# Performance work log

Measured on AMD Instinct MI355X. Metric: run time of the kernel, lower is better.

The kernel has to match this reference:

```python
import jax, jax.numpy as jnp
import numpy as np

EPS_NORM = 1e-12
EPS_BN = 1e-5


def _normalize(x):
    n = jnp.linalg.norm(x, axis=-1, keepdims=True)
    return x / jnp.maximum(n, EPS_NORM)


def _bn_train(x, gamma, beta):
    # BatchNorm2d in training mode: stats over all dims except channel (last)
    mean = jnp.mean(x, axis=(0, 1, 2), keepdims=True)
    var = jnp.var(x, axis=(0, 1, 2), keepdims=True)
    return (x - mean) / jnp.sqrt(var + EPS_BN) * gamma + beta


def setup_inputs() -> dict:
    key = jax.random.key(0)
    ks = jax.random.split(key, 16)
    B, N, K, C = 2, 32768, 16, 64
    Cm = 32  # mlp output channels
    Wn = 16  # weightnet output channels
    xyz = jax.random.normal(ks[0], (B, N, 3), dtype=jnp.float32)
    feats = jax.random.normal(ks[1], (B, N, C), dtype=jnp.float32)
    nei_inds = jax.random.randint(ks[2], (B, N, K), 0, N, dtype=jnp.int32)
    xyz_norm = _normalize(jax.random.normal(ks[3], (B, N, 3), dtype=jnp.float32))
    s = 0.05
    return {
        "xyz": xyz, "feats": feats, "xyz_norm": xyz_norm, "nei_inds": nei_inds,
        # main MLP (1x1 convs, no BN since cfg.BATCH_NORM=False)
        "W_mlp1": jax.random.normal(ks[4], (Cm, C + 3), dtype=jnp.float32) * s,
        "b_mlp1": jnp.zeros((Cm,), dtype=jnp.float32),
        "W_mlp2": jax.random.normal(ks[5], (Cm, Cm), dtype=jnp.float32) * s,
        "b_mlp2": jnp.zeros((Cm,), dtype=jnp.float32),
        # weightnet: 12 -> 8 -> 8 -> 16, each conv1x1 + BN + relu
        "wn_W0": jax.random.normal(ks[6], (8, 12), dtype=jnp.float32) * s,
        "wn_b0": jnp.zeros((8,), dtype=jnp.float32),
        "wn_g0": jnp.ones((8,), dtype=jnp.float32),
        "wn_be0": jnp.zeros((8,), dtype=jnp.float32),
        "wn_W1": jax.random.normal(ks[7], (8, 8), dtype=jnp.float32) * s,
        "wn_b1": jnp.zeros((8,), dtype=jnp.float32),
        "wn_g1": jnp.ones((8,), dtype=jnp.float32),
        "wn_be1": jnp.zeros((8,), dtype=jnp.float32),
        "wn_W2": jax.random.normal(ks[8], (Wn, 8), dtype=jnp.float32) * s,
        "wn_b2": jnp.zeros((Wn,), dtype=jnp.float32),
        "wn_g2": jnp.ones((Wn,), dtype=jnp.float32),
        "wn_be2": jnp.zeros((Wn,), dtype=jnp.float32),
        # final linear: Cm*Wn -> C
        "W_lin": jax.random.normal(ks[9], (C, Cm * Wn), dtype=jnp.float32) * s,
        "b_lin": jnp.zeros((C,), dtype=jnp.float32),
    }


def reference(xyz, feats, xyz_norm, nei_inds,
              W_mlp1, b_mlp1, W_mlp2, b_mlp2,
              wn_W0, wn_b0, wn_g0, wn_be0,
              wn_W1, wn_b1, wn_g1, wn_be1,
              wn_W2, wn_b2, wn_g2, wn_be2,
              W_lin, b_lin):
    B, N, _ = xyz.shape
    K = nei_inds.shape[-1]
    bidx = jnp.arange(B)[:, None, None]
    # gathers
    g_xyz = xyz[bidx, nei_inds]          # [B,N,K,3]
    g_norm = xyz_norm[bidx, nei_inds]    # [B,N,K,3]
    g_feat = feats[bidx, nei_inds]       # [B,N,K,C]
    r_miu = g_xyz - xyz[:, :, None, :]   # localized_xyz
    n_miu = xyz_norm[:, :, None, :]      # [B,N,1,3]
    r_hat = _normalize(r_miu)
    # viewpoint-invariant frame
    dot_nm_rhat = jnp.sum(n_miu * r_hat, axis=-1, keepdims=True)
    v_miu = _normalize(n_miu - dot_nm_rhat * r_hat)
    w_miu = _normalize(jnp.cross(r_hat, v_miu))
    th1 = jnp.sum(g_norm * n_miu, axis=-1, keepdims=True)
    th2 = dot_nm_rhat
    th3 = jnp.sum(r_hat * g_norm, axis=-1, keepdims=True)
    th4 = jnp.sum(r_miu * n_miu, axis=-1, keepdims=True)
    th5 = th3
    th6 = jnp.sum(g_norm * v_miu, axis=-1, keepdims=True)
    th7 = jnp.sum(g_norm * w_miu, axis=-1, keepdims=True)
    th8 = jnp.sum(r_miu * jnp.cross(g_norm, jnp.broadcast_to(n_miu, g_norm.shape)),
                  axis=-1, keepdims=True)
    th9 = jnp.linalg.norm(r_miu, axis=-1, keepdims=True)
    wn_in = jnp.concatenate([th1, th2, th3, th4, th5, th6, th7, th8, th9, r_miu], axis=-1)  # [B,N,K,12]
    # feature MLP (1x1 convs, channels-last)
    h = jnp.concatenate([g_feat, r_miu], axis=-1)  # [B,N,K,C+3]
    h = jax.nn.relu(jnp.einsum('bnkc,oc->bnko', h, W_mlp1) + b_mlp1)
    h = jax.nn.relu(jnp.einsum('bnkc,oc->bnko', h, W_mlp2) + b_mlp2)  # [B,N,K,Cm]
    # weightnet (conv1x1 + BN(train) + relu)
    w = wn_in
    for Wc, bc, g, be in ((wn_W0, wn_b0, wn_g0, wn_be0),
                          (wn_W1, wn_b1, wn_g1, wn_be1),
                          (wn_W2, wn_b2, wn_g2, wn_be2)):
        w = jax.nn.relu(_bn_train(jnp.einsum('bnkc,oc->bnko', w, Wc) + bc, g, be))
    # PointConv aggregation over K: [B,N,Cm,Wn] -> flatten (Cm outer, Wn inner)
    agg = jnp.einsum('bnkc,bnkw->bncw', h, w).reshape(B, N, -1)
    out = jax.nn.relu(agg @ W_lin.T + b_lin) + feats
    return out
```

## Files before the change

### kernel.cpp

```cpp
#include <hip/hip_runtime.h>
#include <math.h>

#define BB 2
#define NN 32768
#define KK 16
#define CC 64
#define MTOT (BB*NN*KK)

typedef short short8 __attribute__((ext_vector_type(8)));
typedef float f32x4 __attribute__((ext_vector_type(4)));

static_assert(MTOT == 1048576, "size");

__device__ __forceinline__ float frsq(float x) { return __builtin_amdgcn_rsqf(x); }

__device__ __forceinline__ unsigned cvtpk(float lo, float hi) {
    unsigned r;
    asm("v_cvt_pk_bf16_f32 %0, %1, %2" : "=v"(r) : "v"(lo), "v"(hi));
    return r;
}

__device__ __forceinline__ short f2bf(float f) {
    union { float f; unsigned u; } c; c.f = f;
    const unsigned r = c.u + 0x7FFFu + ((c.u >> 16) & 1u);
    return (short)(r >> 16);
}

__device__ __forceinline__ float bf2f(unsigned short u) {
    union { unsigned u; float f; } c; c.u = ((unsigned)u) << 16; return c.f;
}

__device__ __forceinline__ f32x4 mfma16(short8 a, short8 b, f32x4 c) {
    return __builtin_amdgcn_mfma_f32_16x16x32_bf16(a, b, c, 0, 0, 0);
}

__device__ __forceinline__ void geom12(int s, const float* __restrict__ xyz,
                                       const float* __restrict__ xyzn,
                                       const int* __restrict__ nei, float* win) {
    const int pn = s >> 4;
    const int b  = pn >> 15;
    const int nj = nei[s];
    const size_t gj = (size_t)(b * NN + nj);

    const float cx = xyz[(size_t)pn*3],  cy = xyz[(size_t)pn*3+1],  cz = xyz[(size_t)pn*3+2];
    const float nmx = xyzn[(size_t)pn*3], nmy = xyzn[(size_t)pn*3+1], nmz = xyzn[(size_t)pn*3+2];
    const float gx = xyz[gj*3],  gy = xyz[gj*3+1],  gz = xyz[gj*3+2];
    const float gnx = xyzn[gj*3], gny = xyzn[gj*3+1], gnz = xyzn[gj*3+2];

    const float rx = gx - cx, ry = gy - cy, rz = gz - cz;
    const float ss = rx*rx + ry*ry + rz*rz;
    const float rinv = frsq(fmaxf(ss, 1e-24f));
    const float rlen = ss * rinv;
    const float rhx = rx*rinv, rhy = ry*rinv, rhz = rz*rinv;

    const float d_nr = nmx*rhx + nmy*rhy + nmz*rhz;
    float vx = nmx - d_nr*rhx, vy = nmy - d_nr*rhy, vz = nmz - d_nr*rhz;
    const float vinv = frsq(fmaxf(vx*vx + vy*vy + vz*vz, 1e-24f));
    vx *= vinv; vy *= vinv; vz *= vinv;

    float wx = rhy*vz - rhz*vy;
    float wy = rhz*vx - rhx*vz;
    float wz = rhx*vy - rhy*vx;
    const float winv = frsq(fmaxf(wx*wx + wy*wy + wz*wz, 1e-24f));
    wx *= winv; wy *= winv; wz *= winv;

    const float th1 = gnx*nmx + gny*nmy + gnz*nmz;
    const float th3 = rhx*gnx + rhy*gny + rhz*gnz;
    const float th4 = rx*nmx + ry*nmy + rz*nmz;
    const float th6 = gnx*vx + gny*vy + gnz*vz;
    const float th7 = gnx*wx + gny*wy + gnz*wz;
    const float ccx = gny*nmz - gnz*nmy;
    const float ccy = gnz*nmx - gnx*nmz;
    const float ccz = gnx*nmy - gny*nmx;
    const float th8 = rx*ccx + ry*ccy + rz*ccz;

    win[0]=th1; win[1]=d_nr; win[2]=th3; win[3]=th4; win[4]=th3; win[5]=th6;
    win[6]=th7; win[7]=th8; win[8]=rlen; win[9]=rx; win[10]=ry; win[11]=rz;
}

template<int ON, int IN>
__device__ __forceinline__ void lin(const float* a, const float* __restrict__ W,
                                    const float* __restrict__ bias, float* z) {
#pragma unroll
    for (int o = 0; o < ON; ++o) {
        float acc = bias[o];
#pragma unroll
        for (int c = 0; c < IN; ++c) acc += a[c] * W[o*IN + c];
        z[o] = acc;
    }
}

template<int NV>
__device__ __forceinline__ void block_reduce_atomic(const float* v, float* gdst) {
    __shared__ float red[NV * 4];
    const int lane = threadIdx.x & 63;
    const int wv   = threadIdx.x >> 6;
    float tmp[NV];
#pragma unroll
    for (int i = 0; i < NV; ++i) {
        float x = v[i];
#pragma unroll
        for (int off = 32; off > 0; off >>= 1) x += __shfl_down(x, off, 64);
        tmp[i] = x;
    }
    if (lane == 0) {
#pragma unroll
        for (int i = 0; i < NV; ++i) red[wv * NV + i] = tmp[i];
    }
    __syncthreads();
    if (threadIdx.x < NV) {
        float s = red[threadIdx.x] + red[NV + threadIdx.x] +
                  red[2*NV + threadIdx.x] + red[3*NV + threadIdx.x];
        atomicAdd(gdst + threadIdx.x, s);
    }
}

__global__ __launch_bounds__(256)
void kA(const float* __restrict__ xyz, const float* __restrict__ xyzn,
        const int* __restrict__ nei, const float* __restrict__ W0,
        const float* __restrict__ b0,
        const float* __restrict__ Wm1, const float* __restrict__ Wm2,
        const float* __restrict__ Wlin, const float* __restrict__ feats,
        unsigned short* __restrict__ z0ws, unsigned short* __restrict__ rmws,
        short* __restrict__ fWm1, short* __restrict__ fWm2,
        short* __restrict__ fWlin, unsigned short* __restrict__ featsbf,
        float* __restrict__ stats) {
    const int t = threadIdx.x;
    const int gid  = blockIdx.x * 256 + t;
    const int gstr = gridDim.x * 256;

    for (int i = gid; i < 3072; i += gstr) {
        const int j = i & 7, l = (i >> 3) & 63, fn = i >> 9;
        const int ks = fn >> 1, nt = fn & 1;
        const int k = ks*32 + ((l >> 4) * 8) + j, n = nt*16 + (l & 15);
        fWm1[i] = (k < 67) ? f2bf(Wm1[n*67 + k]) : (short)0;
    }
    for (int i = gid; i < 1024; i += gstr) {
        const int j = i & 7, l = (i >> 3) & 63, nt = i >> 9;
        const int k = ((l >> 4) * 8) + j, n = nt*16 + (l & 15);
        fWm2[i] = f2bf(Wm2[n*32 + k]);
    }
    for (int i = gid; i < 32768; i += gstr) {
        const int j = i & 7, l = (i >> 3) & 63, fn = i >> 9;
        const int ks = fn >> 2, nt = fn & 3;
        const int k = ks*32 + ((l >> 4) * 8) + j, n = nt*16 + (l & 15);
        fWlin[i] = f2bf(Wlin[n*512 + k]);
    }
    for (int i = gid; i < (BB*NN*CC)/4; i += gstr) {
        const float4 f = *(const float4*)(feats + (size_t)i*4);
        uint2 p; p.x = cvtpk(f.x, f.y); p.y = cvtpk(f.z, f.w);
        *(uint2*)(featsbf + (size_t)i*4) = p;
    }

    float acc[16];
#pragma unroll
    for (int i = 0; i < 16; ++i) acc[i] = 0.f;
#pragma unroll
    for (int i = 0; i < 4; ++i) {
        const int s = blockIdx.x*1024 + i*256 + t;
        float win[12]; geom12(s, xyz, xyzn, nei, win);
        float z0[8];  lin<8,12>(win, W0, b0, z0);
        uint4 zp;
        zp.x = cvtpk(z0[0], z0[1]); zp.y = cvtpk(z0[2], z0[3]);
        zp.z = cvtpk(z0[4], z0[5]); zp.w = cvtpk(z0[6], z0[7]);
        *(uint4*)(z0ws + (size_t)s*8) = zp;
        uint2 rp; rp.x = cvtpk(win[9], win[10]); rp.y = cvtpk(win[11], 0.0f);
        *(uint2*)(rmws + (size_t)s*4) = rp;
#pragma unroll
        for (int o = 0; o < 8; ++o) { acc[o] += z0[o]; acc[8+o] += z0[o]*z0[o]; }
    }
    block_reduce_atomic<16>(acc, stats);
}

__global__ __launch_bounds__(256)
void kB(const unsigned short* __restrict__ z0ws, const float* __restrict__ W1,
        const float* __restrict__ b1, const float* __restrict__ g0,
        const float* __restrict__ be0, const float* __restrict__ stats0,
        float* __restrict__ statsOut) {
    const int t = threadIdx.x;
    const float invM = 1.0f / (float)MTOT;
    float sc0[8], sh0[8];
#pragma unroll
    for (int c = 0; c < 8; ++c) {
        const float m = stats0[c] * invM;
        const float v = stats0[8 + c] * invM - m*m;
        const float s = frsq(v + 1e-5f) * g0[c];
        sc0[c] = s; sh0[c] = be0[c] - m*s;
    }
    float acc[16];
#pragma unroll
    for (int i = 0; i < 16; ++i) acc[i] = 0.f;
#pragma unroll
    for (int i = 0; i < 4; ++i) {
        const int s = blockIdx.x*1024 + i*256 + t;
        const uint4 zz = *(const uint4*)(z0ws + (size_t)s*8);
        const unsigned short* q = (const unsigned short*)&zz;
        float a0[8];
#pragma unroll
        for (int c = 0; c < 8; ++c) a0[c] = fmaxf(bf2f(q[c])*sc0[c] + sh0[c], 0.f);
        float z1[8]; lin<8,8>(a0, W1, b1, z1);
#pragma unroll
        for (int o = 0; o < 8; ++o) { acc[o] += z1[o]; acc[8+o] += z1[o]*z1[o]; }
    }
    block_reduce_atomic<16>(acc, statsOut);
}

__global__ __launch_bounds__(256)
void kC(const unsigned short* __restrict__ z0ws, const float* __restrict__ W1,
        const float* __restrict__ b1, const float* __restrict__ W2,
        const float* __restrict__ b2, const float* __restrict__ g0,
        const float* __restrict__ be0, const float* __restrict__ g1,
        const float* __restrict__ be1, const float* __restrict__ stats0,
        float* __restrict__ statsOut) {
    const int t = threadIdx.x;
    const float invM = 1.0f / (float)MTOT;
    float sc0[8], sh0[8], sc1[8], sh1[8];
#pragma unroll
    for (int c = 0; c < 8; ++c) {
        float m = stats0[c] * invM;
        float v = stats0[8 + c] * invM - m*m;
        float s = frsq(v + 1e-5f) * g0[c];
        sc0[c] = s; sh0[c] = be0[c] - m*s;
        m = stats0[16 + c] * invM;
        v = stats0[24 + c] * invM - m*m;
        s = frsq(v + 1e-5f) * g1[c];
        sc1[c] = s; sh1[c] = be1[c] - m*s;
    }
    float acc[32];
#pragma unroll
    for (int i = 0; i < 32; ++i) acc[i] = 0.f;
#pragma unroll
    for (int i = 0; i < 4; ++i) {
        const int s = blockIdx.x*1024 + i*256 + t;
        const uint4 zz = *(const uint4*)(z0ws + (size_t)s*8);
        const unsigned short* q = (const unsigned short*)&zz;
        float a0[8];
#pragma unroll
        for (int c = 0; c < 8; ++c) a0[c] = fmaxf(bf2f(q[c])*sc0[c] + sh0[c], 0.f);
        float z1[8]; lin<8,8>(a0, W1, b1, z1);
        float a1[8];
#pragma unroll
        for (int c = 0; c < 8; ++c) a1[c] = fmaxf(z1[c]*sc1[c] + sh1[c], 0.f);
        float z2[16]; lin<16,8>(a1, W2, b2, z2);
#pragma unroll
        for (int o = 0; o < 16; ++o) { acc[o] += z2[o]; acc[16+o] += z2[o]*z2[o]; }
    }
    block_reduce_atomic<32>(acc, statsOut);
}

__global__ void k_fin(const float* __restrict__ stats,
                      const float* __restrict__ g0, const float* __restrict__ be0,
                      const float* __restrict__ W1, const float* __restrict__ b1,
                      const float* __restrict__ g1, const float* __restrict__ be1,
                      const float* __restrict__ W2, const float* __restrict__ b2,
                      const float* __restrict__ g2, const float* __restrict__ be2,
                      float* __restrict__ fold) {
    __shared__ float sc[32], sh[32];
    const int t = threadIdx.x;
    const float invM = 1.0f / (float)MTOT;
    if (t < 8) {
        const float m = stats[t]*invM, v = stats[8+t]*invM - m*m;
        const float s = frsq(v + 1e-5f) * g0[t];
        sc[t] = s; sh[t] = be0[t] - m*s;
    } else if (t < 16) {
        const int c = t - 8;
        const float m = stats[16+c]*invM, v = stats[24+c]*invM - m*m;
        const float s = frsq(v + 1e-5f) * g1[c];
        sc[t] = s; sh[t] = be1[c] - m*s;
    } else if (t < 32) {
        const int c = t - 16;
        const float m = stats[32+c]*invM, v = stats[48+c]*invM - m*m;
        const float s = frsq(v + 1e-5f) * g2[c];
        sc[t] = s; sh[t] = be2[c] - m*s;
    }
    __syncthreads();
    if (t < 8)   { fold[t] = sc[t]; fold[8+t] = sh[t]; }
    if (t < 64)  fold[16 + t] = sc[8 + (t >> 3)] * W1[t];
    if (t < 8)   fold[80 + t] = sc[8 + t]*b1[t] + sh[8 + t];
    if (t < 128) fold[88 + t] = sc[16 + (t >> 3)] * W2[t];
    if (t < 16)  fold[216 + t] = sc[16 + t]*b2[t] + sh[16 + t];
}

__global__ __launch_bounds__(256, 3)
void k_fused(const float* __restrict__ feats,
             const unsigned short* __restrict__ featsbf,
             const int* __restrict__ nei,
             const float* __restrict__ bm1, const float* __restrict__ bm2,
             const float* __restrict__ blin, const float* __restrict__ fold,
             const short* __restrict__ fWm1, const short* __restrict__ fWm2,
             const short* __restrict__ fWlin,
             const unsigned short* __restrict__ z0ws,
             const unsigned short* __restrict__ rmws,
             float* __restrict__ out) {
    __shared__ __align__(16) unsigned char smem[46080];
    const int t    = threadIdx.x;
    const int lane = t & 63;
    const int wv   = t >> 6;
    const int blk  = blockIdx.x;
    const int sbase = blk * 256;
    const int b     = (blk >= 2048) ? 1 : 0;
    const int lrow  = lane & 15;
    const int kq    = lane >> 4;

    int njv[4];
#pragma unroll
    for (int mt = 0; mt < 4; ++mt)
        njv[mt] = nei[sbase + wv*64 + mt*16 + lrow];

    const uint4 zz = *(const uint4*)(z0ws + (size_t)(sbase + t)*8);

    short8 bW1[3][2];
#pragma unroll
    for (int ks = 0; ks < 3; ++ks)
#pragma unroll
        for (int nt = 0; nt < 2; ++nt)
            bW1[ks][nt] = *(const short8*)(fWm1 + ((ks*2 + nt)*64 + lane)*8);
    short8 bW2[2];
    bW2[0] = *(const short8*)(fWm2 + (0*64 + lane)*8);
    bW2[1] = *(const short8*)(fWm2 + (1*64 + lane)*8);

    short8 fa[4][2];
    uint2  rmv[4];
#pragma unroll
    for (int mt = 0; mt < 4; ++mt) {
        const unsigned short* F = featsbf + ((size_t)(b*NN + njv[mt])) * CC;
        fa[mt][0] = *(const short8*)(F + kq*8);
        fa[mt][1] = *(const short8*)(F + 32 + kq*8);
        rmv[mt]   = *(const uint2*)(rmws + (size_t)(sbase + wv*64 + mt*16 + lrow)*4);
    }

    {
        const unsigned short* q = (const unsigned short*)&zz;
        float a0[8];
#pragma unroll
        for (int c = 0; c < 8; ++c) a0[c] = fmaxf(bf2f(q[c])*fold[c] + fold[8+c], 0.f);
        float a1[8];
#pragma unroll
        for (int o = 0; o < 8; ++o) {
            float acc = fold[80 + o];
#pragma unroll
            for (int c = 0; c < 8; ++c) acc += a0[c] * fold[16 + o*8 + c];
            a1[o] = fmaxf(acc, 0.f);
        }
        const int p = t >> 4, kk = t & 15;
        unsigned short* WBT = (unsigned short*)(smem + 37376);
#pragma unroll
        for (int o = 0; o < 16; ++o) {
            float acc = fold[216 + o];
#pragma unroll
            for (int c = 0; c < 8; ++c) acc += a1[c] * fold[88 + o*8 + c];
            WBT[p*272 + o*16 + kk] = (unsigned short)f2bf(fmaxf(acc, 0.f));
        }
    }

    {
        f32x4 C1[4][2];
#pragma unroll
        for (int mt = 0; mt < 4; ++mt)
#pragma unroll
            for (int nt = 0; nt < 2; ++nt)
                C1[mt][nt] = (f32x4){0.f, 0.f, 0.f, 0.f};

#pragma unroll
        for (int mt = 0; mt < 4; ++mt) {
            C1[mt][0] = mfma16(fa[mt][0], bW1[0][0], C1[mt][0]);
            C1[mt][1] = mfma16(fa[mt][0], bW1[0][1], C1[mt][1]);
            C1[mt][0] = mfma16(fa[mt][1], bW1[1][0], C1[mt][0]);
            C1[mt][1] = mfma16(fa[mt][1], bW1[1][1], C1[mt][1]);
            short8 ar = (short8){0,0,0,0,0,0,0,0};
            if (kq == 0)
                *(uint2*)&ar = rmv[mt];
            C1[mt][0] = mfma16(ar, bW1[2][0], C1[mt][0]);
            C1[mt][1] = mfma16(ar, bW1[2][1], C1[mt][1]);
        }
        unsigned short* H1 = (unsigned short*)smem;
#pragma unroll
        for (int mt = 0; mt < 4; ++mt)
#pragma unroll
            for (int nt = 0; nt < 2; ++nt) {
                const int c = nt*16 + lrow;
                const float bias = bm1[c];
#pragma unroll
                for (int reg = 0; reg < 4; ++reg) {
                    const int s = wv*64 + mt*16 + kq*4 + reg;
                    H1[s*40 + c] = (unsigned short)f2bf(fmaxf(C1[mt][nt][reg] + bias, 0.f));
                }
            }
    }

    {
        const unsigned short* H1 = (const unsigned short*)smem;
        f32x4 C2[4][2];
#pragma unroll
        for (int mt = 0; mt < 4; ++mt)
#pragma unroll
            for (int nt = 0; nt < 2; ++nt)
                C2[mt][nt] = (f32x4){0.f, 0.f, 0.f, 0.f};
#pragma unroll
        for (int mt = 0; mt < 4; ++mt) {
            const int s = wv*64 + mt*16 + lrow;
            const short8 a = *(const short8*)(H1 + s*40 + kq*8);
            C2[mt][0] = mfma16(a, bW2[0], C2[mt][0]);
            C2[mt][1] = mfma16(a, bW2[1], C2[mt][1]);
        }
        unsigned short* H2T = (unsigned short*)(smem + 20480);
#pragma unroll
        for (int mt = 0; mt < 4; ++mt)
#pragma unroll
            for (int nt = 0; nt < 2; ++nt) {
                const int c = nt*16 + lrow;
                const float bias = bm2[c];
                const int s0 = wv*64 + mt*16 + kq*4;
                const float r0 = fmaxf(C2[mt][nt][0] + bias, 0.f);
                const float r1 = fmaxf(C2[mt][nt][1] + bias, 0.f);
                const float r2 = fmaxf(C2[mt][nt][2] + bias, 0.f);
                const float r3 = fmaxf(C2[mt][nt][3] + bias, 0.f);
                uint2 pk; pk.x = cvtpk(r0, r1); pk.y = cvtpk(r2, r3);
                *(uint2*)&H2T[c*264 + s0] = pk;
            }
    }

    __syncthreads();

    {
        const unsigned short* H2T = (const unsigned short*)(smem + 20480);
        const unsigned short* WBT = (const unsigned short*)(smem + 37376);
        unsigned short* AGG = (unsigned short*)smem;
#pragma unroll
        for (int pi = 0; pi < 4; ++pi) {
            const int p = wv*4 + pi;
            short8 bf = (short8){0,0,0,0,0,0,0,0};
            if (kq < 2)
                bf = *(const short8*)(WBT + p*272 + lrow*16 + kq*8);
#pragma unroll
            for (int ct = 0; ct < 2; ++ct) {
                short8 af = (short8){0,0,0,0,0,0,0,0};
                if (kq < 2) {
                    const int c = ct*16 + lrow;
                    af = *(const short8*)(H2T + c*264 + p*16 + kq*8);
                }
                f32x4 Cg = (f32x4){0.f, 0.f, 0.f, 0.f};
                Cg = mfma16(af, bf, Cg);
#pragma unroll
                for (int reg = 0; reg < 4; ++reg) {
                    const int c = ct*16 + kq*4 + reg;
                    AGG[p*520 + c*16 + lrow] = (unsigned short)f2bf(Cg[reg]);
                }
            }
        }
    }

    __syncthreads();

    {
        const unsigned short* AGG = (const unsigned short*)smem;
        const int nt = wv;
        f32x4 Co = (f32x4){0.f, 0.f, 0.f, 0.f};
#pragma unroll
        for (int ks = 0; ks < 16; ++ks) {
            const short8 a  = *(const short8*)(AGG + lrow*520 + ks*32 + kq*8);
            const short8 bf = *(const short8*)(fWlin + ((ks*4 + nt)*64 + lane)*8);
            Co = mfma16(a, bf, Co);
        }
        const int o = nt*16 + lrow;
        const float bias = blin[o];
#pragma unroll
        for (int reg = 0; reg < 4; ++reg) {
            const int p = kq*4 + reg;
            const size_t gp = (size_t)blk*16 + p;
            out[gp*CC + o] = fmaxf(Co[reg] + bias, 0.f) + feats[gp*CC + o];
        }
    }
}

extern "C" void kernel_launch(void* const* d_in, const int* in_sizes, int n_in,
                              void* d_out, int out_size, void* d_ws, size_t ws_size,
                              hipStream_t stream) {
    const float* xyz  = (const float*)d_in[0];
    const float* feats= (const float*)d_in[1];
    const float* xyzn = (const float*)d_in[2];
    const int*   nei  = (const int*)  d_in[3];
    const float* Wm1  = (const float*)d_in[4];
    const float* bm1  = (const float*)d_in[5];
    const float* Wm2  = (const float*)d_in[6];
    const float* bm2  = (const float*)d_in[7];
    const float* W0   = (const float*)d_in[8];
    const float* b0   = (const float*)d_in[9];
    const float* g0   = (const float*)d_in[10];
    const float* be0  = (const float*)d_in[11];
    const float* W1   = (const float*)d_in[12];
    const float* b1   = (const float*)d_in[13];
    const float* g1   = (const float*)d_in[14];
    const float* be1  = (const float*)d_in[15];
    const float* W2   = (const float*)d_in[16];
    const float* b2   = (const float*)d_in[17];
    const float* g2   = (const float*)d_in[18];
    const float* be2  = (const float*)d_in[19];
    const float* Wlin = (const float*)d_in[20];
    const float* blin = (const float*)d_in[21];

    float* out = (float*)d_out;
    char*  ws  = (char*)d_ws;

    float*          stats   = (float*)ws;
    float*          fold    = (float*)(ws + 256);
    short*          fWm1    = (short*)(ws + 2048);
    short*          fWm2    = (short*)(ws + 8192);
    short*          fWlin   = (short*)(ws + 16384);
    unsigned short* featsbf = (unsigned short*)(ws + 131072);
    unsigned short* z0ws    = (unsigned short*)(ws + 8519680);
    unsigned short* rmws    = (unsigned short*)(ws + 25296896);

    hipMemsetAsync(stats, 0, 256, stream);

    kA<<<1024, 256, 0, stream>>>(xyz, xyzn, nei, W0, b0, Wm1, Wm2, Wlin,
                                 feats, z0ws, rmws, fWm1, fWm2, fWlin,
                                 featsbf, stats);
    kB<<<1024, 256, 0, stream>>>(z0ws, W1, b1, g0, be0, stats, stats + 16);
    kC<<<1024, 256, 0, stream>>>(z0ws, W1, b1, W2, b2, g0, be0, g1, be1,
                                 stats, stats + 32);
    k_fin<<<1, 256, 0, stream>>>(stats, g0, be0, W1, b1, g1, be1,
                                 W2, b2, g2, be2, fold);
    k_fused<<<4096, 256, 0, stream>>>(feats, featsbf, nei, bm1, bm2, blin,
                                      fold, fWm1, fWm2, fWlin, z0ws, rmws, out);
}
```

Before: 124.1 us.

## Merge BN statistics kernels into one persistent kernel with grid barriers

Replaces the four statistics kernels (kA, kB, kC, k_fin) with a single persistent kernel of 512 blocks. Each block keeps its z0 values in registers and crosses phases through software grid barriers built on atomics. This removes three kernel launches and the re-reads of z0 from global memory in the later phases. In exchange it relies on all 512 blocks being co-resident, or the barrier deadlocks, and it raises register pressure to hold 64 floats per thread. Stats are now computed from bf16-rounded z0 values, so they match what the later phases see.

```diff
diff --git a/kernel.cpp b/kernel.cpp
--- a/kernel.cpp
+++ b/kernel.cpp
@@ -6,6 +6,7 @@
 #define KK 16
 #define CC 64
 #define MTOT (BB*NN*KK)
+#define NBLK 512
 
 typedef short short8 __attribute__((ext_vector_type(8)));
 typedef float f32x4 __attribute__((ext_vector_type(4)));
@@ -30,8 +31,23 @@
     union { unsigned u; float f; } c; c.u = ((unsigned)u) << 16; return c.f;
 }
 
+__device__ __forceinline__ float ld_dev(const float* p) {
+    return __hip_atomic_load(p, __ATOMIC_RELAXED, __HIP_MEMORY_SCOPE_AGENT);
+}
+
 __device__ __forceinline__ f32x4 mfma16(short8 a, short8 b, f32x4 c) {
     return __builtin_amdgcn_mfma_f32_16x16x32_bf16(a, b, c, 0, 0, 0);
+}
+
+__device__ __forceinline__ void gsync(int* bar, int target) {
+    __syncthreads();
+    if (threadIdx.x == 0) {
+        __threadfence();
+        __hip_atomic_fetch_add(bar, 1, __ATOMIC_ACQ_REL, __HIP_MEMORY_SCOPE_AGENT);
+        while (__hip_atomic_load(bar, __ATOMIC_ACQUIRE, __HIP_MEMORY_SCOPE_AGENT) < target)
+            __builtin_amdgcn_s_sleep(8);
+    }
+    __syncthreads();
 }
 
 __device__ __forceinline__ void geom12(int s, const float* __restrict__ xyz,
@@ -115,19 +131,26 @@
     }
 }
 
-__global__ __launch_bounds__(256)
-void kA(const float* __restrict__ xyz, const float* __restrict__ xyzn,
-        const int* __restrict__ nei, const float* __restrict__ W0,
-        const float* __restrict__ b0,
-        const float* __restrict__ Wm1, const float* __restrict__ Wm2,
-        const float* __restrict__ Wlin, const float* __restrict__ feats,
-        unsigned short* __restrict__ z0ws, unsigned short* __restrict__ rmws,
-        short* __restrict__ fWm1, short* __restrict__ fWm2,
-        short* __restrict__ fWlin, unsigned short* __restrict__ featsbf,
-        float* __restrict__ stats) {
+__global__ __launch_bounds__(256, 2)
+void k_stats(const float* __restrict__ xyz, const float* __restrict__ xyzn,
+             const int* __restrict__ nei,
+             const float* __restrict__ W0, const float* __restrict__ b0,
+             const float* __restrict__ W1, const float* __restrict__ b1,
+             const float* __restrict__ W2, const float* __restrict__ b2,
+             const float* __restrict__ g0, const float* __restrict__ be0,
+             const float* __restrict__ g1, const float* __restrict__ be1,
+             const float* __restrict__ g2, const float* __restrict__ be2,
+             const float* __restrict__ Wm1, const float* __restrict__ Wm2,
+             const float* __restrict__ Wlin, const float* __restrict__ feats,
+             unsigned short* __restrict__ z0ws, unsigned short* __restrict__ rmws,
+             short* __restrict__ fWm1, short* __restrict__ fWm2,
+             short* __restrict__ fWlin, unsigned short* __restrict__ featsbf,
+             float* __restrict__ stats, int* __restrict__ bar,
+             float* __restrict__ fold) {
     const int t = threadIdx.x;
     const int gid  = blockIdx.x * 256 + t;
-    const int gstr = gridDim.x * 256;
+    const int gstr = NBLK * 256;
+    const float invM = 1.0f / (float)MTOT;
 
     for (int i = gid; i < 3072; i += gstr) {
         const int j = i & 7, l = (i >> 3) & 63, fn = i >> 9;
@@ -152,133 +175,109 @@
         *(uint2*)(featsbf + (size_t)i*4) = p;
     }
 
-    float acc[16];
-#pragma unroll
-    for (int i = 0; i < 16; ++i) acc[i] = 0.f;
-#pragma unroll
-    for (int i = 0; i < 4; ++i) {
-        const int s = blockIdx.x*1024 + i*256 + t;
-        float win[12]; geom12(s, xyz, xyzn, nei, win);
-        float z0[8];  lin<8,12>(win, W0, b0, z0);
-        uint4 zp;
-        zp.x = cvtpk(z0[0], z0[1]); zp.y = cvtpk(z0[2], z0[3]);
-        zp.z = cvtpk(z0[4], z0[5]); zp.w = cvtpk(z0[6], z0[7]);
-        *(uint4*)(z0ws + (size_t)s*8) = zp;
-        uint2 rp; rp.x = cvtpk(win[9], win[10]); rp.y = cvtpk(win[11], 0.0f);
-        *(uint2*)(rmws + (size_t)s*4) = rp;
-#pragma unroll
-        for (int o = 0; o < 8; ++o) { acc[o] += z0[o]; acc[8+o] += z0[o]*z0[o]; }
-    }
-    block_reduce_atomic<16>(acc, stats);
-}
-
-__global__ __launch_bounds__(256)
-void kB(const unsigned short* __restrict__ z0ws, const float* __restrict__ W1,
-        const float* __restrict__ b1, const float* __restrict__ g0,
-        const float* __restrict__ be0, const float* __restrict__ stats0,
-        float* __restrict__ statsOut) {
-    const int t = threadIdx.x;
-    const float invM = 1.0f / (float)MTOT;
+    float z0r[8][8];
+    {
+        float acc[16];
+#pragma unroll
+        for (int i = 0; i < 16; ++i) acc[i] = 0.f;
+#pragma unroll
+        for (int i = 0; i < 8; ++i) {
+            const int s = blockIdx.x*2048 + i*256 + t;
+            float win[12]; geom12(s, xyz, xyzn, nei, win);
+            float z0[8];  lin<8,12>(win, W0, b0, z0);
+            uint4 zp;
+            zp.x = cvtpk(z0[0], z0[1]); zp.y = cvtpk(z0[2], z0[3]);
+            zp.z = cvtpk(z0[4], z0[5]); zp.w = cvtpk(z0[6], z0[7]);
+            *(uint4*)(z0ws + (size_t)s*8) = zp;
+            uint2 rp; rp.x = cvtpk(win[9], win[10]); rp.y = cvtpk(win[11], 0.0f);
+            *(uint2*)(rmws + (size_t)s*4) = rp;
+#pragma unroll
+            for (int c = 0; c < 8; ++c) z0r[i][c] = bf2f((unsigned short)f2bf(z0[c]));
+#pragma unroll
+            for (int o = 0; o < 8; ++o) { acc[o] += z0r[i][o]; acc[8+o] += z0r[i][o]*z0r[i][o]; }
+        }
+        block_reduce_atomic<16>(acc, stats);
+    }
+    gsync(bar, NBLK);
+
     float sc0[8], sh0[8];
-#pragma unroll
-    for (int c = 0; c < 8; ++c) {
-        const float m = stats0[c] * invM;
-        const float v = stats0[8 + c] * invM - m*m;
-        const float s = frsq(v + 1e-5f) * g0[c];
-        sc0[c] = s; sh0[c] = be0[c] - m*s;
-    }
-    float acc[16];
-#pragma unroll
-    for (int i = 0; i < 16; ++i) acc[i] = 0.f;
-#pragma unroll
-    for (int i = 0; i < 4; ++i) {
-        const int s = blockIdx.x*1024 + i*256 + t;
-        const uint4 zz = *(const uint4*)(z0ws + (size_t)s*8);
-        const unsigned short* q = (const unsigned short*)&zz;
-        float a0[8];
-#pragma unroll
-        for (int c = 0; c < 8; ++c) a0[c] = fmaxf(bf2f(q[c])*sc0[c] + sh0[c], 0.f);
-        float z1[8]; lin<8,8>(a0, W1, b1, z1);
-#pragma unroll
-        for (int o = 0; o < 8; ++o) { acc[o] += z1[o]; acc[8+o] += z1[o]*z1[o]; }
-    }
-    block_reduce_atomic<16>(acc, statsOut);
-}
-
-__global__ __launch_bounds__(256)
-void kC(const unsigned short* __restrict__ z0ws, const float* __restrict__ W1,
-        const float* __restrict__ b1, const float* __restrict__ W2,
-        const float* __restrict__ b2, const float* __restrict__ g0,
-        const float* __restrict__ be0, const float* __restrict__ g1,
-        const float* __restrict__ be1, const float* __restrict__ stats0,
-        float* __restrict__ statsOut) {
-    const int t = threadIdx.x;
-    const float invM = 1.0f / (float)MTOT;
-    float sc0[8], sh0[8], sc1[8], sh1[8];
-#pragma unroll
-    for (int c = 0; c < 8; ++c) {
-        float m = stats0[c] * invM;
-        float v = stats0[8 + c] * invM - m*m;
-        float s = frsq(v + 1e-5f) * g0[c];
-        sc0[c] = s; sh0[c] = be0[c] - m*s;
-        m = stats0[16 + c] * invM;
-        v = stats0[24 + c] * invM - m*m;
-        s = frsq(v + 1e-5f) * g1[c];
-        sc1[c] = s; sh1[c] = be1[c] - m*s;
-    }
-    float acc[32];
-#pragma unroll
-    for (int i = 0; i < 32; ++i) acc[i] = 0.f;
-#pragma unroll
-    for (int i = 0; i < 4; ++i) {
-        const int s = blockIdx.x*1024 + i*256 + t;
-        const uint4 zz = *(const uint4*)(z0ws + (size_t)s*8);
-        const unsigned short* q = (const unsigned short*)&zz;
-        float a0[8];
-#pragma unroll
-        for (int c = 0; c < 8; ++c) a0[c] = fmaxf(bf2f(q[c])*sc0[c] + sh0[c], 0.f);
-        float z1[8]; lin<8,8>(a0, W1, b1, z1);
-        float a1[8];
-#pragma unroll
-        for (int c = 0; c < 8; ++c) a1[c] = fmaxf(z1[c]*sc1[c] + sh1[c], 0.f);
-        float z2[16]; lin<16,8>(a1, W2, b2, z2);
-#pragma unroll
-        for (int o = 0; o < 16; ++o) { acc[o] += z2[o]; acc[16+o] += z2[o]*z2[o]; }
-    }
-    block_reduce_atomic<32>(acc, statsOut);
-}
-
-__global__ void k_fin(const float* __restrict__ stats,
-                      const float* __restrict__ g0, const float* __restrict__ be0,
-                      const float* __restrict__ W1, const float* __restrict__ b1,
-                      const float* __restrict__ g1, const float* __restrict__ be1,
-                      const float* __restrict__ W2, const float* __restrict__ b2,
-                      const float* __restrict__ g2, const float* __restrict__ be2,
-                      float* __restrict__ fold) {
-    __shared__ float sc[32], sh[32];
-    const int t = threadIdx.x;
-    const float invM = 1.0f / (float)MTOT;
-    if (t < 8) {
-        const float m = stats[t]*invM, v = stats[8+t]*invM - m*m;
-        const float s = frsq(v + 1e-5f) * g0[t];
-        sc[t] = s; sh[t] = be0[t] - m*s;
-    } else if (t < 16) {
-        const int c = t - 8;
-        const float m = stats[16+c]*invM, v = stats[24+c]*invM - m*m;
-        const float s = frsq(v + 1e-5f) * g1[c];
-        sc[t] = s; sh[t] = be1[c] - m*s;
-    } else if (t < 32) {
-        const int c = t - 16;
-        const float m = stats[32+c]*invM, v = stats[48+c]*invM - m*m;
-        const float s = frsq(v + 1e-5f) * g2[c];
-        sc[t] = s; sh[t] = be2[c] - m*s;
-    }
-    __syncthreads();
-    if (t < 8)   { fold[t] = sc[t]; fold[8+t] = sh[t]; }
-    if (t < 64)  fold[16 + t] = sc[8 + (t >> 3)] * W1[t];
-    if (t < 8)   fold[80 + t] = sc[8 + t]*b1[t] + sh[8 + t];
-    if (t < 128) fold[88 + t] = sc[16 + (t >> 3)] * W2[t];
-    if (t < 16)  fold[216 + t] = sc[16 + t]*b2[t] + sh[16 + t];
+    {
+#pragma unroll
+        for (int c = 0; c < 8; ++c) {
+            const float m = ld_dev(stats + c) * invM;
+            const float v = ld_dev(stats + 8 + c) * invM - m*m;
+            const float s = frsq(v + 1e-5f) * g0[c];
+            sc0[c] = s; sh0[c] = be0[c] - m*s;
+        }
+        float acc[16];
+#pragma unroll
+        for (int i = 0; i < 16; ++i) acc[i] = 0.f;
+#pragma unroll
+        for (int i = 0; i < 8; ++i) {
+            float a0[8];
+#pragma unroll
+            for (int c = 0; c < 8; ++c) a0[c] = fmaxf(z0r[i][c]*sc0[c] + sh0[c], 0.f);
+            float z1[8]; lin<8,8>(a0, W1, b1, z1);
+#pragma unroll
+            for (int o = 0; o < 8; ++o) { acc[o] += z1[o]; acc[8+o] += z1[o]*z1[o]; }
+        }
+        block_reduce_atomic<16>(acc, stats + 16);
+    }
+    gsync(bar, 2*NBLK);
+
+    {
+        float sc1[8], sh1[8];
+#pragma unroll
+        for (int c = 0; c < 8; ++c) {
+            const float m = ld_dev(stats + 16 + c) * invM;
+            const float v = ld_dev(stats + 24 + c) * invM - m*m;
+            const float s = frsq(v + 1e-5f) * g1[c];
+            sc1[c] = s; sh1[c] = be1[c] - m*s;
+        }
+        float acc[32];
+#pragma unroll
+        for (int i = 0; i < 32; ++i) acc[i] = 0.f;
+#pragma unroll
+        for (int i = 0; i < 8; ++i) {
+            float a0[8];
+#pragma unroll
+            for (int c = 0; c < 8; ++c) a0[c] = fmaxf(z0r[i][c]*sc0[c] + sh0[c], 0.f);
+            float z1[8]; lin<8,8>(a0, W1, b1, z1);
+            float a1[8];
+#pragma unroll
+            for (int c = 0; c < 8; ++c) a1[c] = fmaxf(z1[c]*sc1[c] + sh1[c], 0.f);
+            float z2[16]; lin<16,8>(a1, W2, b2, z2);
+#pragma unroll
+            for (int o = 0; o < 16; ++o) { acc[o] += z2[o]; acc[16+o] += z2[o]*z2[o]; }
+        }
+        block_reduce_atomic<32>(acc, stats + 32);
+    }
+    gsync(bar, 3*NBLK);
+
+    if (blockIdx.x == 0) {
+        __shared__ float sc[32], sh[32];
+        if (t < 8) {
+            const float m = ld_dev(stats + t)*invM, v = ld_dev(stats + 8+t)*invM - m*m;
+            const float s = frsq(v + 1e-5f) * g0[t];
+            sc[t] = s; sh[t] = be0[t] - m*s;
+        } else if (t < 16) {
+            const int c = t - 8;
+            const float m = ld_dev(stats + 16+c)*invM, v = ld_dev(stats + 24+c)*invM - m*m;
+            const float s = frsq(v + 1e-5f) * g1[c];
+            sc[t] = s; sh[t] = be1[c] - m*s;
+        } else if (t < 32) {
+            const int c = t - 16;
+            const float m = ld_dev(stats + 32+c)*invM, v = ld_dev(stats + 48+c)*invM - m*m;
+            const float s = frsq(v + 1e-5f) * g2[c];
+            sc[t] = s; sh[t] = be2[c] - m*s;
+        }
+        __syncthreads();
+        if (t < 8)   { fold[t] = sc[t]; fold[8+t] = sh[t]; }
+        if (t < 64)  fold[16 + t] = sc[8 + (t >> 3)] * W1[t];
+        if (t < 8)   fold[80 + t] = sc[8 + t]*b1[t] + sh[8 + t];
+        if (t < 128) fold[88 + t] = sc[16 + (t >> 3)] * W2[t];
+        if (t < 16)  fold[216 + t] = sc[16 + t]*b2[t] + sh[16 + t];
+    }
 }
 
 __global__ __launch_bounds__(256, 3)
@@ -503,7 +502,8 @@
     char*  ws  = (char*)d_ws;
 
     float*          stats   = (float*)ws;
-    float*          fold    = (float*)(ws + 256);
+    int*            bar     = (int*)(ws + 256);
+    float*          fold    = (float*)(ws + 512);
     short*          fWm1    = (short*)(ws + 2048);
     short*          fWm2    = (short*)(ws + 8192);
     short*          fWlin   = (short*)(ws + 16384);
@@ -511,16 +511,13 @@
     unsigned short* z0ws    = (unsigned short*)(ws + 8519680);
     unsigned short* rmws    = (unsigned short*)(ws + 25296896);
 
-    hipMemsetAsync(stats, 0, 256, stream);
-
-    kA<<<1024, 256, 0, stream>>>(xyz, xyzn, nei, W0, b0, Wm1, Wm2, Wlin,
-                                 feats, z0ws, rmws, fWm1, fWm2, fWlin,
-                                 featsbf, stats);
-    kB<<<1024, 256, 0, stream>>>(z0ws, W1, b1, g0, be0, stats, stats + 16);
-    kC<<<1024, 256, 0, stream>>>(z0ws, W1, b1, W2, b2, g0, be0, g1, be1,
-                                 stats, stats + 32);
-    k_fin<<<1, 256, 0, stream>>>(stats, g0, be0, W1, b1, g1, be1,
-                                 W2, b2, g2, be2, fold);
+    hipMemsetAsync(ws, 0, 512, stream);
+
+    k_stats<<<NBLK, 256, 0, stream>>>(xyz, xyzn, nei, W0, b0, W1, b1, W2, b2,
+                                      g0, be0, g1, be1, g2, be2, Wm1, Wm2,
+                                      Wlin, feats, z0ws, rmws, fWm1, fWm2,
+                                      fWlin, featsbf, stats, bar, fold);
+
     k_fused<<<4096, 256, 0, stream>>>(feats, featsbf, nei, bm1, bm2, blin,
                                       fold, fWm1, fWm2, fWlin, z0ws, rmws, out);
 }
```

Result: slower. 253.9 us (+104.6%).
